# Kernel optimization log

Measured on AMD Instinct MI355X. Metric: run time of the kernel, lower is better.

## Reference

```python
import jax, jax.numpy as jnp
import numpy as np

N2, N1, N0 = 16000, 4000, 1000   # leaf / mid / target node counts
DEG = 32                          # sampled neighbors per target
IN_DIM, OUT_DIM, H = 256, 64, 4
NEG = -9e15
ALPHA = 0.2                       # LeakyReLU slope


def setup_inputs() -> dict:
    key = jax.random.key(0)
    ks = jax.random.split(key, 10)
    s = 0.05  # xavier-ish scale
    x = jax.random.normal(ks[0], (N2, IN_DIM), jnp.float32)
    W0 = jax.random.normal(ks[1], (H, IN_DIM, OUT_DIM), jnp.float32) * s
    a0 = jax.random.normal(ks[2], (H, 2 * OUT_DIM), jnp.float32) * s
    W1 = jax.random.normal(ks[3], (H, OUT_DIM * H, OUT_DIM), jnp.float32) * s
    a1 = jax.random.normal(ks[4], (H, 2 * OUT_DIM), jnp.float32) * s
    lin_W = jax.random.normal(ks[5], (OUT_DIM * H, OUT_DIM * H), jnp.float32) * s
    lin_b = jax.random.normal(ks[6], (OUT_DIM * H,), jnp.float32) * s
    # level-1 edges: n1 targets, each with DEG sampled leaf neighbors + self-loop
    adj1_tgt = jnp.concatenate([jnp.repeat(jnp.arange(N1), DEG), jnp.arange(N1)]).astype(jnp.int32)
    adj1_nbr = jnp.concatenate([jax.random.randint(ks[7], (N1 * DEG,), 0, N2),
                                jnp.arange(N1)]).astype(jnp.int32)
    # level-0 edges: n0 targets, each with DEG sampled mid neighbors + self-loop
    adj0_tgt = jnp.concatenate([jnp.repeat(jnp.arange(N0), DEG), jnp.arange(N0)]).astype(jnp.int32)
    adj0_nbr = jnp.concatenate([jax.random.randint(ks[8], (N0 * DEG,), 0, N1),
                                jnp.arange(N0)]).astype(jnp.int32)
    return {"x": x, "W0": W0, "a0": a0, "W1": W1, "a1": a1,
            "lin_W": lin_W, "lin_b": lin_b,
            "adj1_tgt": adj1_tgt, "adj1_nbr": adj1_nbr,
            "adj0_tgt": adj0_tgt, "adj0_nbr": adj0_nbr,
            "n0": N0, "n1": N1}


def _att_layer(x, W, a, tgt, nbr, T):
    # x: [N, D], W: [H, D, O], a: [H, 2O]; multi-head GAT layer (eval mode, no dropout)
    h = jnp.einsum('nd,hdo->hno', x, W)                      # [H, N, O]
    O = h.shape[-1]
    e = jax.nn.leaky_relu(
        jnp.einsum('heo,ho->he', h[:, tgt], a[:, :O]) +
        jnp.einsum('heo,ho->he', h[:, nbr], a[:, O:]), ALPHA)  # [H, E]
    N = h.shape[1]
    att = jnp.full((h.shape[0], T, N), NEG, x.dtype).at[:, tgt, nbr].set(e)
    att = jax.nn.softmax(att, axis=-1)                        # dense edge-softmax
    hp = jax.nn.elu(jnp.einsum('htn,hno->hto', att, h))       # [H, T, O]
    return jnp.transpose(hp, (1, 0, 2)).reshape(T, -1)        # cat heads -> [T, H*O]


def reference(x, W0, a0, W1, a1, lin_W, lin_b,
              adj1_tgt, adj1_nbr, adj0_tgt, adj0_nbr, n0, n1):
    x1 = _att_layer(x, W0, a0, adj1_tgt, adj1_nbr, n1)   # [n1, H*O]
    x2 = _att_layer(x1, W1, a1, adj0_tgt, adj0_nbr, n0)  # [n0, H*O]
    return jnp.tanh(x2 @ lin_W.T + lin_b)                # Linear + Tanh
```

## Files before the change

kernel.cpp:

```cpp
#include <hip/hip_runtime.h>
#include <math.h>

#define N2C 16000
#define N1C 4000
#define N0C 1000
#define DEG 32
#define CH 256
#define NHEAD 4
#define ODIM 64
#define ALPHA 0.2f
#define LDP 264

typedef __attribute__((ext_vector_type(8))) short bf16x8;
typedef __attribute__((ext_vector_type(4))) float f32x4;

__device__ __forceinline__ ushort f2bf(float f) {
    unsigned u = __float_as_uint(f);
    unsigned r = (u + 0x7fffu + ((u >> 16) & 1u)) >> 16;
    return (ushort)r;
}
__device__ __forceinline__ float bf2f(ushort h) {
    return __uint_as_float(((unsigned)h) << 16);
}

__global__ __launch_bounds__(256) void repack_kernel(
    const float* __restrict__ W0, const float* __restrict__ W1,
    const float* __restrict__ linW,
    ushort* __restrict__ Wth, ushort* __restrict__ Wtl)
{
    int g = blockIdx.x * 256 + threadIdx.x;
    int mat = g >> 16;
    int idx = g & 65535;
    int c = idx >> 8, k = idx & 255;
    float v;
    if (mat == 0)      v = W0[(c >> 6) * (256 * 64) + k * 64 + (c & 63)];
    else if (mat == 1) v = W1[(c >> 6) * (256 * 64) + k * 64 + (c & 63)];
    else               v = linW[c * 256 + k];
    ushort h = f2bf(v);
    Wth[g] = h;
    Wtl[g] = f2bf(v - bf2f(h));
}

template<int RT, int EPI, int AF32, int SC>
__global__ __launch_bounds__(256) void gemm_mfma(
    const float* __restrict__ Af,
    const ushort* __restrict__ Ah, const ushort* __restrict__ Al,
    const ushort* __restrict__ Bh, const ushort* __restrict__ Bl,
    const float* __restrict__ bias, const float* __restrict__ avec,
    float* __restrict__ out, float* __restrict__ s_t, float* __restrict__ s_n, int M)
{
    __shared__ ushort sah[AF32 ? RT * 16 * LDP : 1];
    __shared__ ushort sal[AF32 ? RT * 16 * LDP : 1];

    const int wave = threadIdx.x >> 6;
    const int lane = threadIdx.x & 63;
    const int quad = lane >> 4, l16 = lane & 15;
    const int row0 = blockIdx.x * (RT * 16);
    const int col0 = wave * 64;

    if (AF32) {
        for (int idx = threadIdx.x; idx < RT * 16 * 64; idx += 256) {
            int row = idx >> 6, c4 = idx & 63;
            int gr = row0 + row; if (gr >= M) gr = M - 1;
            float4 f = ((const float4*)Af)[gr * 64 + c4];
            ushort4 h, l;
            h.x = f2bf(f.x); l.x = f2bf(f.x - bf2f(h.x));
            h.y = f2bf(f.y); l.y = f2bf(f.y - bf2f(h.y));
            h.z = f2bf(f.z); l.z = f2bf(f.z - bf2f(h.z));
            h.w = f2bf(f.w); l.w = f2bf(f.w - bf2f(h.w));
            *(ushort4*)(&sah[row * LDP + c4 * 4]) = h;
            *(ushort4*)(&sal[row * LDP + c4 * 4]) = l;
        }
        __syncthreads();
    }

    f32x4 acc[RT][4];
#pragma unroll
    for (int r = 0; r < RT; ++r)
#pragma unroll
        for (int c = 0; c < 4; ++c) acc[r][c] = (f32x4){0.f, 0.f, 0.f, 0.f};

    int arow[RT];
#pragma unroll
    for (int r = 0; r < RT; ++r) {
        int rr = row0 + r * 16 + l16;
        arow[r] = (rr < M) ? rr : (M - 1);
    }
    const int kbase = quad * 8;

    for (int k0 = 0; k0 < 256; k0 += 32) {
        bf16x8 a_h[RT], a_l[RT], b_h[4], b_l[4];
#pragma unroll
        for (int r = 0; r < RT; ++r) {
            if (AF32) {
                int loff = (r * 16 + l16) * LDP + k0 + kbase;
                a_h[r] = *(const bf16x8*)(&sah[loff]);
                a_l[r] = *(const bf16x8*)(&sal[loff]);
            } else {
                int off = arow[r] * 256 + k0 + kbase;
                a_h[r] = *(const bf16x8*)(Ah + off);
                a_l[r] = *(const bf16x8*)(Al + off);
            }
        }
#pragma unroll
        for (int c = 0; c < 4; ++c) {
            int off = (col0 + c * 16 + l16) * 256 + k0 + kbase;
            b_h[c] = *(const bf16x8*)(Bh + off);
            b_l[c] = *(const bf16x8*)(Bl + off);
        }
#pragma unroll
        for (int r = 0; r < RT; ++r)
#pragma unroll
            for (int c = 0; c < 4; ++c) {
                acc[r][c] = __builtin_amdgcn_mfma_f32_16x16x32_bf16(a_h[r], b_h[c], acc[r][c], 0, 0, 0);
                acc[r][c] = __builtin_amdgcn_mfma_f32_16x16x32_bf16(a_h[r], b_l[c], acc[r][c], 0, 0, 0);
                acc[r][c] = __builtin_amdgcn_mfma_f32_16x16x32_bf16(a_l[r], b_h[c], acc[r][c], 0, 0, 0);
            }
    }

#pragma unroll
    for (int r = 0; r < RT; ++r)
#pragma unroll
        for (int c = 0; c < 4; ++c) {
            int col = col0 + c * 16 + l16;
#pragma unroll
            for (int reg = 0; reg < 4; ++reg) {
                int row = row0 + r * 16 + quad * 4 + reg;
                if (row < M) {
                    float v = acc[r][c][reg];
                    if (EPI == 1) v = tanhf(v + bias[col]);
                    out[row * 256 + col] = v;
                }
            }
        }

    if (SC) {
        float at[4], an[4];
#pragma unroll
        for (int c = 0; c < 4; ++c) {
            at[c] = avec[wave * 128 + c * 16 + l16];
            an[c] = avec[wave * 128 + 64 + c * 16 + l16];
        }
#pragma unroll
        for (int r = 0; r < RT; ++r) {
            float pt[4] = {0.f, 0.f, 0.f, 0.f}, pn[4] = {0.f, 0.f, 0.f, 0.f};
#pragma unroll
            for (int c = 0; c < 4; ++c)
#pragma unroll
                for (int reg = 0; reg < 4; ++reg) {
                    pt[reg] += acc[r][c][reg] * at[c];
                    pn[reg] += acc[r][c][reg] * an[c];
                }
#pragma unroll
            for (int reg = 0; reg < 4; ++reg)
#pragma unroll
                for (int m = 1; m < 16; m <<= 1) {
                    pt[reg] += __shfl_xor(pt[reg], m);
                    pn[reg] += __shfl_xor(pn[reg], m);
                }
            if (l16 == 0) {
#pragma unroll
                for (int reg = 0; reg < 4; ++reg) {
                    int row = row0 + r * 16 + quad * 4 + reg;
                    if (row < M) {
                        s_t[wave * M + row] = pt[reg];
                        s_n[wave * M + row] = pn[reg];
                    }
                }
            }
        }
    }
}

__global__ __launch_bounds__(256) void att_kernel(
    const float* __restrict__ hprev, const int* __restrict__ nbr_arr,
    const float* __restrict__ s_t, const float* __restrict__ s_n,
    ushort* __restrict__ outhi, ushort* __restrict__ outlo, int T, int Nsrc)
{
    __shared__ int nbr[DEG + 1];
    __shared__ float att_s[NHEAD][DEG + 3];
    __shared__ float4 red[4][64];
    const int tgt = blockIdx.x;
    const int t = threadIdx.x;
    const int lane = t & 63;
    if (t < DEG) nbr[t] = nbr_arr[tgt * DEG + t];
    else if (t == DEG) nbr[DEG] = nbr_arr[T * DEG + tgt];
    __syncthreads();

    {
        const int hd = t >> 6;
        int me = (lane <= DEG) ? nbr[lane] : -1;
        int k = (lane <= DEG) ? 1 : 0;
#pragma unroll
        for (int j = 0; j < DEG; ++j) {
            int v = __shfl(me, j);
            if (j < lane && v == me) k = 0;
        }
        float e = s_t[hd * Nsrc + tgt] + ((lane <= DEG) ? s_n[hd * Nsrc + me] : 0.f);
        e = (e >= 0.f) ? e : ALPHA * e;
        float em = k ? e : -1e30f;
        float m = em;
#pragma unroll
        for (int off = 1; off < 64; off <<= 1) m = fmaxf(m, __shfl_xor(m, off));
        float w = k ? __expf(e - m) : 0.f;
        float Z = w;
#pragma unroll
        for (int off = 1; off < 64; off <<= 1) Z += __shfl_xor(Z, off);
        if (lane <= DEG) att_s[hd][lane] = w / Z;
    }
    __syncthreads();

    const int cq = t & 63;
    const int rg = t >> 6;
    const int hd = cq >> 4;
    const float4* hp4 = (const float4*)hprev;
    float4 acc = make_float4(0.f, 0.f, 0.f, 0.f);
#pragma unroll
    for (int ii = 0; ii < 9; ++ii) {
        int i = rg + ii * 4;
        if (i <= DEG) {
            float w = att_s[hd][i];
            float4 v = hp4[(size_t)nbr[i] * 64 + cq];
            acc.x += w * v.x; acc.y += w * v.y;
            acc.z += w * v.z; acc.w += w * v.w;
        }
    }
    red[rg][cq] = acc;
    __syncthreads();
    if (t < 64) {
        float4 s0 = red[0][t], s1 = red[1][t], s2 = red[2][t], s3 = red[3][t];
        float4 s;
        s.x = s0.x + s1.x + s2.x + s3.x;
        s.y = s0.y + s1.y + s2.y + s3.y;
        s.z = s0.z + s1.z + s2.z + s3.z;
        s.w = s0.w + s1.w + s2.w + s3.w;
        s.x = (s.x > 0.f) ? s.x : expm1f(s.x);
        s.y = (s.y > 0.f) ? s.y : expm1f(s.y);
        s.z = (s.z > 0.f) ? s.z : expm1f(s.z);
        s.w = (s.w > 0.f) ? s.w : expm1f(s.w);
        ushort4 h, l;
        h.x = f2bf(s.x); l.x = f2bf(s.x - bf2f(h.x));
        h.y = f2bf(s.y); l.y = f2bf(s.y - bf2f(h.y));
        h.z = f2bf(s.z); l.z = f2bf(s.z - bf2f(h.z));
        h.w = f2bf(s.w); l.w = f2bf(s.w - bf2f(h.w));
        ((ushort4*)outhi)[tgt * 64 + t] = h;
        ((ushort4*)outlo)[tgt * 64 + t] = l;
    }
}

extern "C" void kernel_launch(void* const* d_in, const int* in_sizes, int n_in,
                              void* d_out, int out_size, void* d_ws, size_t ws_size,
                              hipStream_t stream)
{
    const float* x    = (const float*)d_in[0];
    const float* W0   = (const float*)d_in[1];
    const float* a0   = (const float*)d_in[2];
    const float* W1   = (const float*)d_in[3];
    const float* a1   = (const float*)d_in[4];
    const float* linW = (const float*)d_in[5];
    const float* linb = (const float*)d_in[6];
    const int* adj1_nbr = (const int*)d_in[8];
    const int* adj0_nbr = (const int*)d_in[10];

    char* base = (char*)d_ws;
    ushort* Wth = (ushort*)base;
    ushort* Wtl = Wth + 3 * 65536;
    float*  st  = (float*)(base + 786432);
    float*  sn  = st + 65536;
    float*  h0  = (float*)(base + 1310720);
    ushort* xhi = (ushort*)(base + 1310720 + 16384000);
    ushort* xlo = xhi + 4096000;

    repack_kernel<<<768, 256, 0, stream>>>(W0, W1, linW, Wth, Wtl);

    gemm_mfma<2, 0, 1, 1><<<N2C / 32, 256, 0, stream>>>(
        x, nullptr, nullptr, Wth, Wtl, nullptr, a0, h0, st, sn, N2C);
    att_kernel<<<N1C, 256, 0, stream>>>(h0, adj1_nbr, st, sn, xhi, xlo, N1C, N2C);

    gemm_mfma<1, 0, 0, 1><<<N1C / 16, 256, 0, stream>>>(
        nullptr, xhi, xlo, Wth + 65536, Wtl + 65536, nullptr, a1, h0, st, sn, N1C);
    att_kernel<<<N0C, 256, 0, stream>>>(h0, adj0_nbr, st, sn, xhi, xlo, N0C, N1C);

    gemm_mfma<1, 1, 0, 0><<<(N0C + 15) / 16, 256, 0, stream>>>(
        nullptr, xhi, xlo, Wth + 131072, Wtl + 131072, linb, nullptr,
        (float*)d_out, nullptr, nullptr, N0C);
}
```

Baseline: 167.2 us.

## Fuse attention aggregation with following GEMM and final linear layer

Merges each attention-aggregation step with the next projection. Layer-1 attention now writes its bf16 hi/lo output into shared memory and feeds MFMA directly, and layer-0 attention is fused with the final linear plus tanh using a scalar dot product. This removes two kernel launches and the global round-trips of the intermediate hi/lo activations. It also adds nontemporal stores and specialises the kernels to fixed sizes. The risk is lower parallelism: each block aggregates 16 targets sequentially, and the last stage has only 250 blocks doing scalar FMA work.

```diff
diff --git a/kernel.cpp b/kernel.cpp
--- a/kernel.cpp
+++ b/kernel.cpp
@@ -5,9 +5,7 @@
 #define N1C 4000
 #define N0C 1000
 #define DEG 32
-#define CH 256
 #define NHEAD 4
-#define ODIM 64
 #define ALPHA 0.2f
 #define LDP 264
 
@@ -37,70 +35,50 @@
     else if (mat == 1) v = W1[(c >> 6) * (256 * 64) + k * 64 + (c & 63)];
     else               v = linW[c * 256 + k];
     ushort h = f2bf(v);
-    Wth[g] = h;
-    Wtl[g] = f2bf(v - bf2f(h));
-}
-
-template<int RT, int EPI, int AF32, int SC>
-__global__ __launch_bounds__(256) void gemm_mfma(
+    __builtin_nontemporal_store(h, &Wth[g]);
+    __builtin_nontemporal_store(f2bf(v - bf2f(h)), &Wtl[g]);
+}
+
+__global__ __launch_bounds__(256) void gemm1_kernel(
     const float* __restrict__ Af,
-    const ushort* __restrict__ Ah, const ushort* __restrict__ Al,
     const ushort* __restrict__ Bh, const ushort* __restrict__ Bl,
-    const float* __restrict__ bias, const float* __restrict__ avec,
-    float* __restrict__ out, float* __restrict__ s_t, float* __restrict__ s_n, int M)
-{
-    __shared__ ushort sah[AF32 ? RT * 16 * LDP : 1];
-    __shared__ ushort sal[AF32 ? RT * 16 * LDP : 1];
-
-    const int wave = threadIdx.x >> 6;
-    const int lane = threadIdx.x & 63;
+    const float* __restrict__ avec,
+    float* __restrict__ out, float* __restrict__ s_t, float* __restrict__ s_n)
+{
+    __shared__ ushort sah[32 * LDP];
+    __shared__ ushort sal[32 * LDP];
+    const int wave = threadIdx.x >> 6, lane = threadIdx.x & 63;
     const int quad = lane >> 4, l16 = lane & 15;
-    const int row0 = blockIdx.x * (RT * 16);
+    const int row0 = blockIdx.x * 32;
     const int col0 = wave * 64;
 
-    if (AF32) {
-        for (int idx = threadIdx.x; idx < RT * 16 * 64; idx += 256) {
-            int row = idx >> 6, c4 = idx & 63;
-            int gr = row0 + row; if (gr >= M) gr = M - 1;
-            float4 f = ((const float4*)Af)[gr * 64 + c4];
-            ushort4 h, l;
-            h.x = f2bf(f.x); l.x = f2bf(f.x - bf2f(h.x));
-            h.y = f2bf(f.y); l.y = f2bf(f.y - bf2f(h.y));
-            h.z = f2bf(f.z); l.z = f2bf(f.z - bf2f(h.z));
-            h.w = f2bf(f.w); l.w = f2bf(f.w - bf2f(h.w));
-            *(ushort4*)(&sah[row * LDP + c4 * 4]) = h;
-            *(ushort4*)(&sal[row * LDP + c4 * 4]) = l;
-        }
-        __syncthreads();
-    }
-
-    f32x4 acc[RT][4];
-#pragma unroll
-    for (int r = 0; r < RT; ++r)
+    for (int idx = threadIdx.x; idx < 32 * 64; idx += 256) {
+        int row = idx >> 6, c4 = idx & 63;
+        float4 f = ((const float4*)Af)[(size_t)(row0 + row) * 64 + c4];
+        ushort4 h, l;
+        h.x = f2bf(f.x); l.x = f2bf(f.x - bf2f(h.x));
+        h.y = f2bf(f.y); l.y = f2bf(f.y - bf2f(h.y));
+        h.z = f2bf(f.z); l.z = f2bf(f.z - bf2f(h.z));
+        h.w = f2bf(f.w); l.w = f2bf(f.w - bf2f(h.w));
+        *(ushort4*)(&sah[row * LDP + c4 * 4]) = h;
+        *(ushort4*)(&sal[row * LDP + c4 * 4]) = l;
+    }
+    __syncthreads();
+
+    f32x4 acc[2][4];
+#pragma unroll
+    for (int r = 0; r < 2; ++r)
 #pragma unroll
         for (int c = 0; c < 4; ++c) acc[r][c] = (f32x4){0.f, 0.f, 0.f, 0.f};
-
-    int arow[RT];
-#pragma unroll
-    for (int r = 0; r < RT; ++r) {
-        int rr = row0 + r * 16 + l16;
-        arow[r] = (rr < M) ? rr : (M - 1);
-    }
     const int kbase = quad * 8;
 
     for (int k0 = 0; k0 < 256; k0 += 32) {
-        bf16x8 a_h[RT], a_l[RT], b_h[4], b_l[4];
-#pragma unroll
-        for (int r = 0; r < RT; ++r) {
-            if (AF32) {
-                int loff = (r * 16 + l16) * LDP + k0 + kbase;
-                a_h[r] = *(const bf16x8*)(&sah[loff]);
-                a_l[r] = *(const bf16x8*)(&sal[loff]);
-            } else {
-                int off = arow[r] * 256 + k0 + kbase;
-                a_h[r] = *(const bf16x8*)(Ah + off);
-                a_l[r] = *(const bf16x8*)(Al + off);
-            }
+        bf16x8 a_h[2], a_l[2], b_h[4], b_l[4];
+#pragma unroll
+        for (int r = 0; r < 2; ++r) {
+            int loff = (r * 16 + l16) * LDP + k0 + kbase;
+            a_h[r] = *(const bf16x8*)(&sah[loff]);
+            a_l[r] = *(const bf16x8*)(&sal[loff]);
         }
 #pragma unroll
         for (int c = 0; c < 4; ++c) {
@@ -109,7 +87,7 @@
             b_l[c] = *(const bf16x8*)(Bl + off);
         }
 #pragma unroll
-        for (int r = 0; r < RT; ++r)
+        for (int r = 0; r < 2; ++r)
 #pragma unroll
             for (int c = 0; c < 4; ++c) {
                 acc[r][c] = __builtin_amdgcn_mfma_f32_16x16x32_bf16(a_h[r], b_h[c], acc[r][c], 0, 0, 0);
@@ -119,133 +97,270 @@
     }
 
 #pragma unroll
-    for (int r = 0; r < RT; ++r)
+    for (int r = 0; r < 2; ++r)
 #pragma unroll
         for (int c = 0; c < 4; ++c) {
             int col = col0 + c * 16 + l16;
 #pragma unroll
             for (int reg = 0; reg < 4; ++reg) {
                 int row = row0 + r * 16 + quad * 4 + reg;
-                if (row < M) {
-                    float v = acc[r][c][reg];
-                    if (EPI == 1) v = tanhf(v + bias[col]);
-                    out[row * 256 + col] = v;
-                }
-            }
-        }
-
-    if (SC) {
-        float at[4], an[4];
-#pragma unroll
-        for (int c = 0; c < 4; ++c) {
-            at[c] = avec[wave * 128 + c * 16 + l16];
-            an[c] = avec[wave * 128 + 64 + c * 16 + l16];
-        }
-#pragma unroll
-        for (int r = 0; r < RT; ++r) {
-            float pt[4] = {0.f, 0.f, 0.f, 0.f}, pn[4] = {0.f, 0.f, 0.f, 0.f};
-#pragma unroll
-            for (int c = 0; c < 4; ++c)
-#pragma unroll
-                for (int reg = 0; reg < 4; ++reg) {
-                    pt[reg] += acc[r][c][reg] * at[c];
-                    pn[reg] += acc[r][c][reg] * an[c];
-                }
-#pragma unroll
-            for (int reg = 0; reg < 4; ++reg)
-#pragma unroll
-                for (int m = 1; m < 16; m <<= 1) {
-                    pt[reg] += __shfl_xor(pt[reg], m);
-                    pn[reg] += __shfl_xor(pn[reg], m);
-                }
-            if (l16 == 0) {
-#pragma unroll
-                for (int reg = 0; reg < 4; ++reg) {
-                    int row = row0 + r * 16 + quad * 4 + reg;
-                    if (row < M) {
-                        s_t[wave * M + row] = pt[reg];
-                        s_n[wave * M + row] = pn[reg];
-                    }
-                }
-            }
-        }
-    }
-}
-
-__global__ __launch_bounds__(256) void att_kernel(
-    const float* __restrict__ hprev, const int* __restrict__ nbr_arr,
+                __builtin_nontemporal_store(acc[r][c][reg], &out[(size_t)row * 256 + col]);
+            }
+        }
+
+    float at[4], an[4];
+#pragma unroll
+    for (int c = 0; c < 4; ++c) {
+        at[c] = avec[wave * 128 + c * 16 + l16];
+        an[c] = avec[wave * 128 + 64 + c * 16 + l16];
+    }
+#pragma unroll
+    for (int r = 0; r < 2; ++r) {
+        float pt[4] = {0.f, 0.f, 0.f, 0.f}, pn[4] = {0.f, 0.f, 0.f, 0.f};
+#pragma unroll
+        for (int c = 0; c < 4; ++c)
+#pragma unroll
+            for (int reg = 0; reg < 4; ++reg) {
+                pt[reg] += acc[r][c][reg] * at[c];
+                pn[reg] += acc[r][c][reg] * an[c];
+            }
+#pragma unroll
+        for (int reg = 0; reg < 4; ++reg)
+#pragma unroll
+            for (int m = 1; m < 16; m <<= 1) {
+                pt[reg] += __shfl_xor(pt[reg], m);
+                pn[reg] += __shfl_xor(pn[reg], m);
+            }
+        if (l16 == 0) {
+#pragma unroll
+            for (int reg = 0; reg < 4; ++reg) {
+                int row = row0 + r * 16 + quad * 4 + reg;
+                __builtin_nontemporal_store(pt[reg], &s_t[wave * N2C + row]);
+                __builtin_nontemporal_store(pn[reg], &s_n[wave * N2C + row]);
+            }
+        }
+    }
+}
+
+__global__ __launch_bounds__(256) void att_gemm_kernel(
+    const float* __restrict__ h0, const int* __restrict__ nbr_arr,
     const float* __restrict__ s_t, const float* __restrict__ s_n,
-    ushort* __restrict__ outhi, ushort* __restrict__ outlo, int T, int Nsrc)
-{
-    __shared__ int nbr[DEG + 1];
-    __shared__ float att_s[NHEAD][DEG + 3];
-    __shared__ float4 red[4][64];
-    const int tgt = blockIdx.x;
-    const int t = threadIdx.x;
-    const int lane = t & 63;
-    if (t < DEG) nbr[t] = nbr_arr[tgt * DEG + t];
-    else if (t == DEG) nbr[DEG] = nbr_arr[T * DEG + tgt];
-    __syncthreads();
-
-    {
-        const int hd = t >> 6;
-        int me = (lane <= DEG) ? nbr[lane] : -1;
+    const ushort* __restrict__ Bh, const ushort* __restrict__ Bl,
+    const float* __restrict__ avec,
+    float* __restrict__ h1, float* __restrict__ st2, float* __restrict__ sn2)
+{
+    __shared__ ushort sah[16 * LDP];
+    __shared__ ushort sal[16 * LDP];
+    __shared__ int   nbr_s[16][DEG + 1];
+    __shared__ float att_w[16][NHEAD][DEG + 1];
+
+    const int wave = threadIdx.x >> 6, lane = threadIdx.x & 63;
+    const int quad = lane >> 4, l16 = lane & 15;
+    const int row0 = blockIdx.x * 16;
+
+    for (int idx = threadIdx.x; idx < 16 * (DEG + 1); idx += 256) {
+        int tt = idx / (DEG + 1), e = idx - tt * (DEG + 1);
+        nbr_s[tt][e] = (e < DEG) ? nbr_arr[(row0 + tt) * DEG + e]
+                                 : nbr_arr[N1C * DEG + row0 + tt];
+    }
+    __syncthreads();
+
+    for (int i = 0; i < 4; ++i) {
+        const int tl = wave * 4 + i;
+        const int gt = row0 + tl;
+        int me = (lane <= DEG) ? nbr_s[tl][lane] : 0;
         int k = (lane <= DEG) ? 1 : 0;
 #pragma unroll
         for (int j = 0; j < DEG; ++j) {
             int v = __shfl(me, j);
             if (j < lane && v == me) k = 0;
         }
-        float e = s_t[hd * Nsrc + tgt] + ((lane <= DEG) ? s_n[hd * Nsrc + me] : 0.f);
-        e = (e >= 0.f) ? e : ALPHA * e;
-        float em = k ? e : -1e30f;
-        float m = em;
-#pragma unroll
-        for (int off = 1; off < 64; off <<= 1) m = fmaxf(m, __shfl_xor(m, off));
-        float w = k ? __expf(e - m) : 0.f;
-        float Z = w;
-#pragma unroll
-        for (int off = 1; off < 64; off <<= 1) Z += __shfl_xor(Z, off);
-        if (lane <= DEG) att_s[hd][lane] = w / Z;
-    }
-    __syncthreads();
-
-    const int cq = t & 63;
-    const int rg = t >> 6;
-    const int hd = cq >> 4;
-    const float4* hp4 = (const float4*)hprev;
-    float4 acc = make_float4(0.f, 0.f, 0.f, 0.f);
-#pragma unroll
-    for (int ii = 0; ii < 9; ++ii) {
-        int i = rg + ii * 4;
-        if (i <= DEG) {
-            float w = att_s[hd][i];
-            float4 v = hp4[(size_t)nbr[i] * 64 + cq];
+#pragma unroll
+        for (int hd = 0; hd < NHEAD; ++hd) {
+            float e = s_t[hd * N2C + gt] + s_n[hd * N2C + me];
+            e = (e >= 0.f) ? e : ALPHA * e;
+            float em = k ? e : -1e30f;
+            float m = em;
+#pragma unroll
+            for (int off = 1; off < 64; off <<= 1) m = fmaxf(m, __shfl_xor(m, off));
+            float w = k ? __expf(e - m) : 0.f;
+            float Z = w;
+#pragma unroll
+            for (int off = 1; off < 64; off <<= 1) Z += __shfl_xor(Z, off);
+            if (lane <= DEG) att_w[tl][hd][lane] = w / Z;
+        }
+        __syncthreads();
+
+        const int hh = lane >> 4;
+        float4 acc = make_float4(0.f, 0.f, 0.f, 0.f);
+#pragma unroll
+        for (int e = 0; e <= DEG; ++e) {
+            float w = att_w[tl][hh][e];
+            float4 v = ((const float4*)h0)[(size_t)nbr_s[tl][e] * 64 + lane];
             acc.x += w * v.x; acc.y += w * v.y;
             acc.z += w * v.z; acc.w += w * v.w;
         }
-    }
-    red[rg][cq] = acc;
-    __syncthreads();
-    if (t < 64) {
-        float4 s0 = red[0][t], s1 = red[1][t], s2 = red[2][t], s3 = red[3][t];
-        float4 s;
-        s.x = s0.x + s1.x + s2.x + s3.x;
-        s.y = s0.y + s1.y + s2.y + s3.y;
-        s.z = s0.z + s1.z + s2.z + s3.z;
-        s.w = s0.w + s1.w + s2.w + s3.w;
-        s.x = (s.x > 0.f) ? s.x : expm1f(s.x);
-        s.y = (s.y > 0.f) ? s.y : expm1f(s.y);
-        s.z = (s.z > 0.f) ? s.z : expm1f(s.z);
-        s.w = (s.w > 0.f) ? s.w : expm1f(s.w);
-        ushort4 h, l;
-        h.x = f2bf(s.x); l.x = f2bf(s.x - bf2f(h.x));
-        h.y = f2bf(s.y); l.y = f2bf(s.y - bf2f(h.y));
-        h.z = f2bf(s.z); l.z = f2bf(s.z - bf2f(h.z));
-        h.w = f2bf(s.w); l.w = f2bf(s.w - bf2f(h.w));
-        ((ushort4*)outhi)[tgt * 64 + t] = h;
-        ((ushort4*)outlo)[tgt * 64 + t] = l;
-    }
+        acc.x = (acc.x > 0.f) ? acc.x : expm1f(acc.x);
+        acc.y = (acc.y > 0.f) ? acc.y : expm1f(acc.y);
+        acc.z = (acc.z > 0.f) ? acc.z : expm1f(acc.z);
+        acc.w = (acc.w > 0.f) ? acc.w : expm1f(acc.w);
+        ushort4 h4, l4;
+        h4.x = f2bf(acc.x); l4.x = f2bf(acc.x - bf2f(h4.x));
+        h4.y = f2bf(acc.y); l4.y = f2bf(acc.y - bf2f(h4.y));
+        h4.z = f2bf(acc.z); l4.z = f2bf(acc.z - bf2f(h4.z));
+        h4.w = f2bf(acc.w); l4.w = f2bf(acc.w - bf2f(h4.w));
+        *(ushort4*)(&sah[tl * LDP + lane * 4]) = h4;
+        *(ushort4*)(&sal[tl * LDP + lane * 4]) = l4;
+    }
+    __syncthreads();
+
+    f32x4 acc2[4];
+#pragma unroll
+    for (int c = 0; c < 4; ++c) acc2[c] = (f32x4){0.f, 0.f, 0.f, 0.f};
+    const int col0 = wave * 64;
+    const int kbase = quad * 8;
+    for (int k0 = 0; k0 < 256; k0 += 32) {
+        bf16x8 a_h, a_l, b_h[4], b_l[4];
+        int loff = l16 * LDP + k0 + kbase;
+        a_h = *(const bf16x8*)(&sah[loff]);
+        a_l = *(const bf16x8*)(&sal[loff]);
+#pragma unroll
+        for (int c = 0; c < 4; ++c) {
+            int off = (col0 + c * 16 + l16) * 256 + k0 + kbase;
+            b_h[c] = *(const bf16x8*)(Bh + off);
+            b_l[c] = *(const bf16x8*)(Bl + off);
+        }
+#pragma unroll
+        for (int c = 0; c < 4; ++c) {
+            acc2[c] = __builtin_amdgcn_mfma_f32_16x16x32_bf16(a_h, b_h[c], acc2[c], 0, 0, 0);
+            acc2[c] = __builtin_amdgcn_mfma_f32_16x16x32_bf16(a_h, b_l[c], acc2[c], 0, 0, 0);
+            acc2[c] = __builtin_amdgcn_mfma_f32_16x16x32_bf16(a_l, b_h[c], acc2[c], 0, 0, 0);
+        }
+    }
+#pragma unroll
+    for (int c = 0; c < 4; ++c) {
+        int col = col0 + c * 16 + l16;
+#pragma unroll
+        for (int reg = 0; reg < 4; ++reg) {
+            int row = row0 + quad * 4 + reg;
+            __builtin_nontemporal_store(acc2[c][reg], &h1[(size_t)row * 256 + col]);
+        }
+    }
+
+    float at[4], an[4];
+#pragma unroll
+    for (int c = 0; c < 4; ++c) {
+        at[c] = avec[wave * 128 + c * 16 + l16];
+        an[c] = avec[wave * 128 + 64 + c * 16 + l16];
+    }
+    float pt[4] = {0.f, 0.f, 0.f, 0.f}, pn[4] = {0.f, 0.f, 0.f, 0.f};
+#pragma unroll
+    for (int c = 0; c < 4; ++c)
+#pragma unroll
+        for (int reg = 0; reg < 4; ++reg) {
+            pt[reg] += acc2[c][reg] * at[c];
+            pn[reg] += acc2[c][reg] * an[c];
+        }
+#pragma unroll
+    for (int reg = 0; reg < 4; ++reg)
+#pragma unroll
+        for (int m = 1; m < 16; m <<= 1) {
+            pt[reg] += __shfl_xor(pt[reg], m);
+            pn[reg] += __shfl_xor(pn[reg], m);
+        }
+    if (l16 == 0) {
+#pragma unroll
+        for (int reg = 0; reg < 4; ++reg) {
+            int row = row0 + quad * 4 + reg;
+            __builtin_nontemporal_store(pt[reg], &st2[wave * N1C + row]);
+            __builtin_nontemporal_store(pn[reg], &sn2[wave * N1C + row]);
+        }
+    }
+}
+
+__global__ __launch_bounds__(256) void att_lin_kernel(
+    const float* __restrict__ h1, const int* __restrict__ nbr_arr,
+    const float* __restrict__ s_t, const float* __restrict__ s_n,
+    const ushort* __restrict__ Bh, const ushort* __restrict__ Bl,
+    const float* __restrict__ bias, float* __restrict__ out)
+{
+    __shared__ int   nbr_s[4][DEG + 1];
+    __shared__ float att_w[4][NHEAD][DEG + 1];
+    __shared__ float x2[4][256];
+
+    const int wave = threadIdx.x >> 6, lane = threadIdx.x & 63;
+    const int blk = blockIdx.x;
+
+    for (int idx = threadIdx.x; idx < 4 * (DEG + 1); idx += 256) {
+        int tt = idx / (DEG + 1), e = idx - tt * (DEG + 1);
+        nbr_s[tt][e] = (e < DEG) ? nbr_arr[(blk * 4 + tt) * DEG + e]
+                                 : nbr_arr[N0C * DEG + blk * 4 + tt];
+    }
+    __syncthreads();
+
+    {
+        const int tl = wave;
+        const int gt = blk * 4 + tl;
+        int me = (lane <= DEG) ? nbr_s[tl][lane] : 0;
+        int k = (lane <= DEG) ? 1 : 0;
+#pragma unroll
+        for (int j = 0; j < DEG; ++j) {
+            int v = __shfl(me, j);
+            if (j < lane && v == me) k = 0;
+        }
+#pragma unroll
+        for (int hd = 0; hd < NHEAD; ++hd) {
+            float e = s_t[hd * N1C + gt] + s_n[hd * N1C + me];
+            e = (e >= 0.f) ? e : ALPHA * e;
+            float em = k ? e : -1e30f;
+            float m = em;
+#pragma unroll
+            for (int off = 1; off < 64; off <<= 1) m = fmaxf(m, __shfl_xor(m, off));
+            float w = k ? __expf(e - m) : 0.f;
+            float Z = w;
+#pragma unroll
+            for (int off = 1; off < 64; off <<= 1) Z += __shfl_xor(Z, off);
+            if (lane <= DEG) att_w[tl][hd][lane] = w / Z;
+        }
+    }
+    __syncthreads();
+    {
+        const int tl = wave;
+        const int hh = lane >> 4;
+        float4 acc = make_float4(0.f, 0.f, 0.f, 0.f);
+#pragma unroll
+        for (int e = 0; e <= DEG; ++e) {
+            float w = att_w[tl][hh][e];
+            float4 v = ((const float4*)h1)[(size_t)nbr_s[tl][e] * 64 + lane];
+            acc.x += w * v.x; acc.y += w * v.y;
+            acc.z += w * v.z; acc.w += w * v.w;
+        }
+        acc.x = (acc.x > 0.f) ? acc.x : expm1f(acc.x);
+        acc.y = (acc.y > 0.f) ? acc.y : expm1f(acc.y);
+        acc.z = (acc.z > 0.f) ? acc.z : expm1f(acc.z);
+        acc.w = (acc.w > 0.f) ? acc.w : expm1f(acc.w);
+        *(float4*)(&x2[tl][lane * 4]) = acc;
+    }
+    __syncthreads();
+
+    const int c = threadIdx.x;
+    float v0 = 0.f, v1 = 0.f, v2 = 0.f, v3 = 0.f;
+    for (int k8 = 0; k8 < 32; ++k8) {
+        bf16x8 hb = *(const bf16x8*)(Bh + c * 256 + k8 * 8);
+        bf16x8 lb = *(const bf16x8*)(Bl + c * 256 + k8 * 8);
+#pragma unroll
+        for (int j = 0; j < 8; ++j) {
+            float wv = bf2f((ushort)hb[j]) + bf2f((ushort)lb[j]);
+            int kk = k8 * 8 + j;
+            v0 += x2[0][kk] * wv; v1 += x2[1][kk] * wv;
+            v2 += x2[2][kk] * wv; v3 += x2[3][kk] * wv;
+        }
+    }
+    float b = bias[c];
+    out[(size_t)(blk * 4 + 0) * 256 + c] = tanhf(v0 + b);
+    out[(size_t)(blk * 4 + 1) * 256 + c] = tanhf(v1 + b);
+    out[(size_t)(blk * 4 + 2) * 256 + c] = tanhf(v2 + b);
+    out[(size_t)(blk * 4 + 3) * 256 + c] = tanhf(v3 + b);
 }
 
 extern "C" void kernel_launch(void* const* d_in, const int* in_sizes, int n_in,
@@ -266,22 +381,19 @@
     ushort* Wth = (ushort*)base;
     ushort* Wtl = Wth + 3 * 65536;
     float*  st  = (float*)(base + 786432);
-    float*  sn  = st + 65536;
-    float*  h0  = (float*)(base + 1310720);
-    ushort* xhi = (ushort*)(base + 1310720 + 16384000);
-    ushort* xlo = xhi + 4096000;
+    float*  sn  = (float*)(base + 1048576);
+    float*  st2 = (float*)(base + 1310720);
+    float*  sn2 = (float*)(base + 1376256);
+    float*  h0  = (float*)(base + 1441792);
+    float*  h1  = (float*)(base + 17825792);
 
     repack_kernel<<<768, 256, 0, stream>>>(W0, W1, linW, Wth, Wtl);
 
-    gemm_mfma<2, 0, 1, 1><<<N2C / 32, 256, 0, stream>>>(
-        x, nullptr, nullptr, Wth, Wtl, nullptr, a0, h0, st, sn, N2C);
-    att_kernel<<<N1C, 256, 0, stream>>>(h0, adj1_nbr, st, sn, xhi, xlo, N1C, N2C);
-
-    gemm_mfma<1, 0, 0, 1><<<N1C / 16, 256, 0, stream>>>(
-        nullptr, xhi, xlo, Wth + 65536, Wtl + 65536, nullptr, a1, h0, st, sn, N1C);
-    att_kernel<<<N0C, 256, 0, stream>>>(h0, adj0_nbr, st, sn, xhi, xlo, N0C, N1C);
-
-    gemm_mfma<1, 1, 0, 0><<<(N0C + 15) / 16, 256, 0, stream>>>(
-        nullptr, xhi, xlo, Wth + 131072, Wtl + 131072, linb, nullptr,
-        (float*)d_out, nullptr, nullptr, N0C);
-}
+    gemm1_kernel<<<N2C / 32, 256, 0, stream>>>(x, Wth, Wtl, a0, h0, st, sn);
+
+    att_gemm_kernel<<<N1C / 16, 256, 0, stream>>>(
+        h0, adj1_nbr, st, sn, Wth + 65536, Wtl + 65536, a1, h1, st2, sn2);
+
+    att_lin_kernel<<<N0C / 4, 256, 0, stream>>>(
+        h1, adj0_nbr, st2, sn2, Wth + 131072, Wtl + 131072, linb, (float*)d_out);
+}
```

Result: slower. 175.9 us (+5.3%).
